# Kernel optimization log

Measured on AMD Instinct MI355X. Metric: run time of the kernel, lower is better.

The kernel has to match this reference:

```python
import math
import jax, jax.numpy as jnp
import numpy as np

WH, WW = 7, 7
NUM_HEADS = 16


def _relative_position_index(wh, ww):
    # Static int index table, identical to the torch buffer construction.
    ch, cw = np.arange(wh), np.arange(ww)
    coords = np.stack(np.meshgrid(ch, cw, indexing='ij'))        # (2, wh, ww)
    cf = coords.reshape(2, -1)                                    # (2, N)
    rel = cf[:, :, None] - cf[:, None, :]                         # (2, N, N)
    rel = rel.transpose(1, 2, 0).copy()                           # (N, N, 2)
    rel[:, :, 0] += wh - 1
    rel[:, :, 1] += ww - 1
    rel[:, :, 0] *= 2 * ww - 1
    return rel.sum(-1)                                            # (N, N) int


def setup_inputs() -> dict:
    key = jax.random.key(0)
    ks = jax.random.split(key, 7)
    B_, N, C = 2048, WH * WW, 512
    nW = 64
    s = 1.0 / math.sqrt(C)
    return {
        'x': jax.random.normal(ks[0], (B_, N, C), jnp.float32),
        'mask': jax.random.normal(ks[1], (nW, N, N), jnp.float32),
        'qkv_w': jax.random.normal(ks[2], (3 * C, C), jnp.float32) * s,
        'qkv_b': jax.random.normal(ks[3], (3 * C,), jnp.float32) * 0.02,
        'proj_w': jax.random.normal(ks[4], (C, C), jnp.float32) * s,
        'proj_b': jax.random.normal(ks[5], (C,), jnp.float32) * 0.02,
        'bias_table': jax.random.normal(ks[6], (2 * WH - 1, 2 * WW - 1, NUM_HEADS), jnp.float32) * 0.02,
    }


def reference(x, mask, qkv_w, qkv_b, proj_w, proj_b, bias_table):
    B_, N, C = x.shape
    nH = NUM_HEADS
    hd = C // nH
    scale = math.sqrt(hd)  # self.scale = qk_scale or sqrt(head_dim)

    qkv = x @ qkv_w.T + qkv_b                                   # (B_, N, 3C)
    qkv = qkv.reshape(B_, N, 3, nH, hd).transpose(2, 0, 3, 1, 4)  # (3, B_, nH, N, hd)
    q, k, v = qkv[0], qkv[1], qkv[2]

    attn = jnp.einsum('bhnd,bhmd->bhnm', q, k) / scale           # (B_, nH, N, N)

    idx = _relative_position_index(WH, WW).reshape(-1)            # (N*N,) static
    bias = bias_table.reshape(-1, nH)[idx].reshape(N, N, nH)      # gather
    attn = attn + bias.transpose(2, 0, 1)[None]                   # (B_, nH, N, N)

    nW = mask.shape[0]
    attn = attn.reshape(B_ // nW, nW, nH, N, N) + mask[None, :, None]
    attn = attn.reshape(B_, nH, N, N)

    attn = jax.nn.softmax(attn, axis=-1)
    out = jnp.einsum('bhnm,bhmd->bhnd', attn, v)                  # (B_, nH, N, hd)
    out = out.transpose(0, 2, 1, 3).reshape(B_, N, C)
    return out @ proj_w.T + proj_b
```

## Files before the change

### kernel.cpp

```cpp
#include <hip/hip_runtime.h>
#include <hip/hip_bf16.h>


typedef __bf16  bf16x8 __attribute__((ext_vector_type(8)));
typedef float   f32x4  __attribute__((ext_vector_type(4)));

#define B_TOT   2048
#define NTOK    49
#define CDIM    512
#define NHEAD   16
#define HDIM    32
#define MROWS   (B_TOT * NTOK)
#define QKVN    (3 * CDIM)

__device__ __forceinline__ void load_lds16(const void* gptr, void* lptr) {
    __builtin_amdgcn_global_load_lds(
        (const __attribute__((address_space(1))) unsigned int*)gptr,
        (__attribute__((address_space(3))) unsigned int*)lptr,
        16, 0, 0);
}
__device__ __forceinline__ void load_lds4(const void* gptr, void* lptr) {
    __builtin_amdgcn_global_load_lds(
        (const __attribute__((address_space(1))) unsigned int*)gptr,
        (__attribute__((address_space(3))) unsigned int*)lptr,
        4, 0, 0);
}

__global__ void cvt_f32_bf16(const float* __restrict__ in,
                             __hip_bfloat16* __restrict__ out, int n4) {
    int idx = blockIdx.x * blockDim.x + threadIdx.x;
    int stride = gridDim.x * blockDim.x;
    for (int i = idx; i < n4; i += stride) {
        float4 f = ((const float4*)in)[i];
        union { __hip_bfloat16 h[4]; ushort4 u; } c;
        c.h[0] = __float2bfloat16(f.x);
        c.h[1] = __float2bfloat16(f.y);
        c.h[2] = __float2bfloat16(f.z);
        c.h[3] = __float2bfloat16(f.w);
        ((ushort4*)out)[i] = c.u;
    }
}

template <typename OutT>
__global__ __launch_bounds__(256) void gemm_bt(
    const __hip_bfloat16* __restrict__ A,
    const __hip_bfloat16* __restrict__ B,
    const float* __restrict__ bias,
    OutT* __restrict__ C,
    int M, int N, int K)
{
    __shared__ __align__(16) __hip_bfloat16 As[128 * 32];
    __shared__ __align__(16) __hip_bfloat16 Bs[128 * 32];

    const int tid  = threadIdx.x;
    const int lane = tid & 63;
    const int wave = tid >> 6;
    const int wm   = (wave >> 1) * 64;
    const int wn   = (wave & 1) * 64;
    const int quad = lane >> 4;
    const int l16  = lane & 15;

    const int m0 = blockIdx.y * 128;
    const int n0 = blockIdx.x * 128;

    const int off0 = tid * 8;
    const int off1 = (256 + tid) * 8;
    const int r0 = off0 >> 5, c0 = off0 & 31;
    const int r1 = off1 >> 5, c1 = off1 & 31;

    const __hip_bfloat16* Ab = A + (long)m0 * K;
    const __hip_bfloat16* Bb = B + (long)n0 * K;

    f32x4 acc[4][4] = {};

    for (int k0 = 0; k0 < K; k0 += 32) {
        load_lds16(Ab + (long)r0 * K + k0 + c0, &As[off0]);
        load_lds16(Ab + (long)r1 * K + k0 + c1, &As[off1]);
        load_lds16(Bb + (long)r0 * K + k0 + c0, &Bs[off0]);
        load_lds16(Bb + (long)r1 * K + k0 + c1, &Bs[off1]);
        __syncthreads();

        bf16x8 a[4], b[4];
#pragma unroll
        for (int i = 0; i < 4; ++i)
            a[i] = *(const bf16x8*)&As[(wm + i * 16 + l16) * 32 + quad * 8];
#pragma unroll
        for (int j = 0; j < 4; ++j)
            b[j] = *(const bf16x8*)&Bs[(wn + j * 16 + l16) * 32 + quad * 8];
#pragma unroll
        for (int i = 0; i < 4; ++i)
#pragma unroll
            for (int j = 0; j < 4; ++j)
                acc[i][j] = __builtin_amdgcn_mfma_f32_16x16x32_bf16(
                    a[i], b[j], acc[i][j], 0, 0, 0);
        __syncthreads();
    }

#pragma unroll
    for (int i = 0; i < 4; ++i) {
#pragma unroll
        for (int j = 0; j < 4; ++j) {
            const int col = n0 + wn + j * 16 + l16;
            const float bv = bias[col];
#pragma unroll
            for (int r = 0; r < 4; ++r) {
                const int row = m0 + wm + i * 16 + quad * 4 + r;
                const float val = acc[i][j][r] + bv;
                if constexpr (sizeof(OutT) == 2)
                    C[(long)row * N + col] = __float2bfloat16(val);
                else
                    C[(long)row * N + col] = val;
            }
        }
    }
}

#define QS_OFF   0
#define KS_OFF   12544
#define VS_OFF   25088
#define BIAS_OFF 41472
#define MASK_OFF 42824
#define SMEM_BYTES 52432

__global__ __launch_bounds__(256) void attn_mfma(
    const __hip_bfloat16* __restrict__ qkv,
    const float* __restrict__ mask,
    const float* __restrict__ bias_table,
    __hip_bfloat16* __restrict__ out)
{
    __shared__ __align__(16) char smem[SMEM_BYTES];

    const int tid  = threadIdx.x;
    const int lane = tid & 63;
    const int w    = tid >> 6;
    const int l16  = lane & 15;
    const int quad = lane >> 4;
    const int b    = blockIdx.x >> 2;
    const int hq   = blockIdx.x & 3;

    {
        const long rowbase = (long)b * NTOK * QKVN;
        for (int e = tid; e < 2352; e += 256) {
            const int m   = e / 784;
            const int rr  = e - m * 784;
            const int tok = rr >> 4, seg = rr & 15;
            const int segl = seg ^ (tok & 7);
            const __hip_bfloat16* src =
                qkv + rowbase + (long)tok * QKVN + m * 512 + hq * 128 + segl * 8;
            load_lds16(src, smem + e * 16);
        }
        for (int e = tid; e < 960; e += 256)
            ((unsigned int*)(smem + VS_OFF + 49 * 256))[e] = 0u;
        const float* msrc = mask + (long)(b & 63) * (NTOK * NTOK);
        for (int e = tid; e < NTOK * NTOK; e += 256)
            load_lds4(msrc + e, smem + MASK_OFF + e * 4);
        __hip_bfloat16* sb = (__hip_bfloat16*)(smem + BIAS_OFF);
        for (int e = tid; e < 676; e += 256) {
            const int w2 = e / 169, rel = e - w2 * 169;
            sb[e] = __float2bfloat16(bias_table[rel * NHEAD + hq * 4 + w2]);
        }
    }
    __syncthreads();

    const int fro = (w * 64 + quad * 16) ^ ((l16 & 7) << 4);
    bf16x8 af[4], bf[4];
#pragma unroll
    for (int t = 0; t < 4; ++t) {
        const int tok = t * 16 + l16;
        af[t] = *(const bf16x8*)(smem + KS_OFF + tok * 256 + fro);
        bf[t] = *(const bf16x8*)(smem + QS_OFF + tok * 256 + fro);
    }
    f32x4 acc[4][4] = {};
#pragma unroll
    for (int i = 0; i < 4; ++i)
#pragma unroll
        for (int j = 0; j < 4; ++j)
            acc[i][j] = __builtin_amdgcn_mfma_f32_16x16x32_bf16(
                af[i], bf[j], acc[i][j], 0, 0, 0);
    __syncthreads();

    const float scale = 0.17677669529663687f;
    const float* smf = (const float*)(smem + MASK_OFF);
    const __hip_bfloat16* sb = (const __hip_bfloat16*)(smem + BIAS_OFF);
    const int quad4 = quad * 4;

    int kp[4][4];
#pragma unroll
    for (int i = 0; i < 4; ++i)
#pragma unroll
        for (int r = 0; r < 4; ++r) {
            const int k  = i * 16 + quad4 + r;
            const int rj = k / 7, cj = k - rj * 7;
            kp[i][r] = (6 - rj) * 13 + (6 - cj);
        }

    char* pbase = smem + w * 6272;
#pragma unroll
    for (int j = 0; j < 4; ++j) {
        const int q   = j * 16 + l16;
        const bool qok = q < NTOK;
        const int ri  = q / 7, ci = q - ri * 7;
        const int qp  = ri * 13 + ci;
        const int mrow = q * NTOK;
        float mx = -1e30f;
#pragma unroll
        for (int i = 0; i < 4; ++i)
#pragma unroll
            for (int r = 0; r < 4; ++r) {
                const int k = i * 16 + quad4 + r;
                float v;
                if (qok && k < NTOK) {
                    v = fmaf(acc[i][j][r], scale,
                             __bfloat162float(sb[w * 169 + qp + kp[i][r]]) + smf[mrow + k]);
                } else {
                    v = -1e30f;
                }
                acc[i][j][r] = v;
                mx = fmaxf(mx, v);
            }
        mx = fmaxf(mx, __shfl_xor(mx, 16));
        mx = fmaxf(mx, __shfl_xor(mx, 32));
        float s = 0.f;
#pragma unroll
        for (int i = 0; i < 4; ++i)
#pragma unroll
            for (int r = 0; r < 4; ++r) {
                const float ev = __expf(acc[i][j][r] - mx);
                acc[i][j][r] = ev;
                s += ev;
            }
        s += __shfl_xor(s, 16);
        s += __shfl_xor(s, 32);
        const float inv = 1.0f / s;
        if (qok) {
            char* prow = pbase + q * 128;
            const int xr = (q & 7) << 4;
#pragma unroll
            for (int i = 0; i < 4; ++i) {
                union { __hip_bfloat16 h[4]; uint2 u; } pk;
#pragma unroll
                for (int r = 0; r < 4; ++r)
                    pk.h[r] = __float2bfloat16(acc[i][j][r] * inv);
                *(uint2*)(prow + ((i * 32 + quad * 8) ^ xr)) = pk.u;
            }
        }
    }
    __syncthreads();

    bf16x8 pa[4][2];
#pragma unroll
    for (int mt = 0; mt < 4; ++mt) {
        const int q  = mt * 16 + l16;
        const int xr = (q & 7) << 4;
#pragma unroll
        for (int ks = 0; ks < 2; ++ks)
            pa[mt][ks] = *(const bf16x8*)(pbase + q * 128 + ((ks * 64 + quad * 16) ^ xr));
    }
    bf16x8 vb[2][2];
#pragma unroll
    for (int dt = 0; dt < 2; ++dt)
#pragma unroll
        for (int ks = 0; ks < 2; ++ks)
#pragma unroll
            for (int e = 0; e < 8; ++e) {
                const int key = ks * 32 + quad * 8 + e;
                const int dby = (w * 32 + dt * 16 + l16) * 2;
                vb[dt][ks][e] = *(const __bf16*)(smem + VS_OFF + key * 256 + (dby ^ (e << 4)));
            }
    f32x4 o[4][2] = {};
#pragma unroll
    for (int mt = 0; mt < 4; ++mt)
#pragma unroll
        for (int dt = 0; dt < 2; ++dt)
#pragma unroll
            for (int ks = 0; ks < 2; ++ks)
                o[mt][dt] = __builtin_amdgcn_mfma_f32_16x16x32_bf16(
                    pa[mt][ks], vb[dt][ks], o[mt][dt], 0, 0, 0);

    const long obase = (long)b * NTOK * CDIM + hq * 128 + w * 32;
#pragma unroll
    for (int mt = 0; mt < 4; ++mt)
#pragma unroll
        for (int r = 0; r < 4; ++r) {
            const int q = mt * 16 + quad4 + r;
            if (q < NTOK) {
                const long rb = obase + (long)q * CDIM;
#pragma unroll
                for (int dt = 0; dt < 2; ++dt)
                    out[rb + dt * 16 + l16] = __float2bfloat16(o[mt][dt][r]);
            }
        }
}

extern "C" void kernel_launch(void* const* d_in, const int* in_sizes, int n_in,
                              void* d_out, int out_size, void* d_ws, size_t ws_size,
                              hipStream_t stream) {
    const float* x          = (const float*)d_in[0];
    const float* mask       = (const float*)d_in[1];
    const float* qkv_w      = (const float*)d_in[2];
    const float* qkv_b      = (const float*)d_in[3];
    const float* proj_w     = (const float*)d_in[4];
    const float* proj_b     = (const float*)d_in[5];
    const float* bias_table = (const float*)d_in[6];

    char* ws = (char*)d_ws;
    __hip_bfloat16* xb   = (__hip_bfloat16*)(ws);
    __hip_bfloat16* qw   = (__hip_bfloat16*)(ws + 102760448);
    __hip_bfloat16* pw   = (__hip_bfloat16*)(ws + 104333312);
    __hip_bfloat16* qkvb = (__hip_bfloat16*)(ws + 104857600);
    __hip_bfloat16* ao   = xb;

    cvt_f32_bf16<<<32768, 256, 0, stream>>>(x, xb, (MROWS * CDIM) / 4);
    cvt_f32_bf16<<<768,   256, 0, stream>>>(qkv_w, qw, (QKVN * CDIM) / 4);
    cvt_f32_bf16<<<256,   256, 0, stream>>>(proj_w, pw, (CDIM * CDIM) / 4);

    gemm_bt<__hip_bfloat16><<<dim3(QKVN / 128, MROWS / 128), 256, 0, stream>>>(
        xb, qw, qkv_b, qkvb, MROWS, QKVN, CDIM);

    attn_mfma<<<B_TOT * 4, 256, 0, stream>>>(qkvb, mask, bias_table, ao);

    gemm_bt<float><<<dim3(CDIM / 128, MROWS / 128), 256, 0, stream>>>(
        ao, pw, proj_b, (float*)d_out, MROWS, CDIM, CDIM);
}
```

Baseline: 795.4 us.

## Replace GEMM with 256x256-tile, double-buffered, ping-pong scheduled MFMA kernel

Replaces the 128x128 single-buffered GEMM with a 512-thread kernel that computes 256x256 tiles over K-steps of 64. Global-to-LDS loads are split into half-tiles and staged into a double buffer, interleaved with MFMA phases using explicit vmcnt waits, barriers and setprio so loads overlap compute. Block IDs are swizzled across 8 groups for L2 locality, and the kernel uses 128KB of dynamic LDS. The aim is less barrier and load stall time and more data reuse per tile, at the cost of high register and LDS use (two blocks per CU) and fragile hand-written wait counts.

```diff
diff --git a/kernel.cpp b/kernel.cpp
--- a/kernel.cpp
+++ b/kernel.cpp
@@ -41,75 +41,151 @@
     }
 }
 
+#define BARR    asm volatile("s_barrier" ::: "memory")
+#define WAITV(N) asm volatile("s_waitcnt vmcnt(" #N ")" ::: "memory")
+#define MFMA16(av, bv, cv) __builtin_amdgcn_mfma_f32_16x16x32_bf16(av, bv, cv, 0, 0, 0)
+
 template <typename OutT>
-__global__ __launch_bounds__(256) void gemm_bt(
+__global__ __launch_bounds__(512, 2) void gemm256(
     const __hip_bfloat16* __restrict__ A,
     const __hip_bfloat16* __restrict__ B,
     const float* __restrict__ bias,
     OutT* __restrict__ C,
-    int M, int N, int K)
+    int M, int N, int K, int nbx, int cpx)
 {
-    __shared__ __align__(16) __hip_bfloat16 As[128 * 32];
-    __shared__ __align__(16) __hip_bfloat16 Bs[128 * 32];
+    extern __shared__ __align__(16) char smem[];
+    char* sA = smem;
+    char* sB = smem + 65536;
+
+    const int NT = K >> 6;
 
     const int tid  = threadIdx.x;
     const int lane = tid & 63;
     const int wave = tid >> 6;
-    const int wm   = (wave >> 1) * 64;
-    const int wn   = (wave & 1) * 64;
+    const int wm   = wave >> 2;
+    const int wn   = wave & 3;
+    const int l16  = lane & 15;
     const int quad = lane >> 4;
-    const int l16  = lane & 15;
-
-    const int m0 = blockIdx.y * 128;
-    const int n0 = blockIdx.x * 128;
-
-    const int off0 = tid * 8;
-    const int off1 = (256 + tid) * 8;
-    const int r0 = off0 >> 5, c0 = off0 & 31;
-    const int r1 = off1 >> 5, c1 = off1 & 31;
-
-    const __hip_bfloat16* Ab = A + (long)m0 * K;
-    const __hip_bfloat16* Bb = B + (long)n0 * K;
-
-    f32x4 acc[4][4] = {};
-
-    for (int k0 = 0; k0 < K; k0 += 32) {
-        load_lds16(Ab + (long)r0 * K + k0 + c0, &As[off0]);
-        load_lds16(Ab + (long)r1 * K + k0 + c1, &As[off1]);
-        load_lds16(Bb + (long)r0 * K + k0 + c0, &Bs[off0]);
-        load_lds16(Bb + (long)r1 * K + k0 + c1, &Bs[off1]);
-        __syncthreads();
-
-        bf16x8 a[4], b[4];
-#pragma unroll
-        for (int i = 0; i < 4; ++i)
-            a[i] = *(const bf16x8*)&As[(wm + i * 16 + l16) * 32 + quad * 8];
-#pragma unroll
-        for (int j = 0; j < 4; ++j)
-            b[j] = *(const bf16x8*)&Bs[(wn + j * 16 + l16) * 32 + quad * 8];
-#pragma unroll
-        for (int i = 0; i < 4; ++i)
-#pragma unroll
-            for (int j = 0; j < 4; ++j)
-                acc[i][j] = __builtin_amdgcn_mfma_f32_16x16x32_bf16(
-                    a[i], b[j], acc[i][j], 0, 0, 0);
-        __syncthreads();
-    }
-
-#pragma unroll
-    for (int i = 0; i < 4; ++i) {
-#pragma unroll
-        for (int j = 0; j < 4; ++j) {
-            const int col = n0 + wn + j * 16 + l16;
+
+    const int id = blockIdx.x;
+    const int sw = (id & 7) * cpx + (id >> 3);
+    const int mb = sw / nbx;
+    const int nb = sw - mb * nbx;
+    const int m0 = mb << 8;
+    const int n0 = nb << 8;
+
+    const int r  = tid >> 2;
+    const int ch = tid & 3;
+    const __hip_bfloat16* Ag0 = A + (size_t)(m0 + r) * K + ch * 8;
+    const __hip_bfloat16* Ag1 = Ag0 + (size_t)128 * K;
+    const __hip_bfloat16* Bg0 = B + (size_t)(n0 + r) * K + ch * 8;
+    const __hip_bfloat16* Bg1 = Bg0 + (size_t)128 * K;
+    char* dA = sA + tid * 16;
+    char* dB = sB + tid * 16;
+
+#define STAGE_A(t2, kh) \
+    { load_lds16(Ag0 + (t2) * 64 + (kh) * 32, dA + ((t2) & 1) * 32768 + (kh) * 16384);        \
+      load_lds16(Ag1 + (t2) * 64 + (kh) * 32, dA + ((t2) & 1) * 32768 + (kh) * 16384 + 8192); }
+#define STAGE_B(t2, kh) \
+    { load_lds16(Bg0 + (t2) * 64 + (kh) * 32, dB + ((t2) & 1) * 32768 + (kh) * 16384);        \
+      load_lds16(Bg1 + (t2) * 64 + (kh) * 32, dB + ((t2) & 1) * 32768 + (kh) * 16384 + 8192); }
+
+    STAGE_A(0, 0); STAGE_B(0, 0);
+    STAGE_A(0, 1); STAGE_B(0, 1);
+    STAGE_A(1, 0); STAGE_B(1, 0);
+    WAITV(8);
+    BARR;
+
+    const int tA = (wm * 128 + l16) * 64 + quad * 16;
+    const int tB = (wn * 64  + l16) * 64 + quad * 16;
+
+    f32x4 acc[8][4] = {};
+    bf16x8 a[8], b[2];
+
+#pragma unroll 2
+    for (int t = 0; t < NT; ++t) {
+        const int sl = (t & 1) * 32768;
+        const char* pA0 = sA + sl;
+        const char* pB0 = sB + sl;
+        const char* pA1 = sA + sl + 16384;
+        const char* pB1 = sB + sl + 16384;
+
+#pragma unroll
+        for (int i = 0; i < 8; ++i) a[i] = *(const bf16x8*)(pA0 + tA + i * 1024);
+        b[0] = *(const bf16x8*)(pB0 + tB);
+        b[1] = *(const bf16x8*)(pB0 + tB + 1024);
+        if (t + 1 < NT) STAGE_A(t + 1, 1);
+        BARR;
+        __builtin_amdgcn_s_setprio(1);
+#pragma unroll
+        for (int i = 0; i < 8; ++i) {
+            acc[i][0] = MFMA16(a[i], b[0], acc[i][0]);
+            acc[i][1] = MFMA16(a[i], b[1], acc[i][1]);
+        }
+        __builtin_amdgcn_s_setprio(0);
+        BARR;
+
+        b[0] = *(const bf16x8*)(pB0 + tB + 2048);
+        b[1] = *(const bf16x8*)(pB0 + tB + 3072);
+        if (t + 1 < NT) STAGE_B(t + 1, 1);
+        BARR;
+        __builtin_amdgcn_s_setprio(1);
+#pragma unroll
+        for (int i = 0; i < 8; ++i) {
+            acc[i][2] = MFMA16(a[i], b[0], acc[i][2]);
+            acc[i][3] = MFMA16(a[i], b[1], acc[i][3]);
+        }
+        __builtin_amdgcn_s_setprio(0);
+        if (t < NT - 1) { WAITV(8); } else { WAITV(0); }
+        BARR;
+
+#pragma unroll
+        for (int i = 0; i < 8; ++i) a[i] = *(const bf16x8*)(pA1 + tA + i * 1024);
+        b[0] = *(const bf16x8*)(pB1 + tB);
+        b[1] = *(const bf16x8*)(pB1 + tB + 1024);
+        if (t + 2 < NT) STAGE_A(t + 2, 0);
+        BARR;
+        __builtin_amdgcn_s_setprio(1);
+#pragma unroll
+        for (int i = 0; i < 8; ++i) {
+            acc[i][0] = MFMA16(a[i], b[0], acc[i][0]);
+            acc[i][1] = MFMA16(a[i], b[1], acc[i][1]);
+        }
+        __builtin_amdgcn_s_setprio(0);
+        BARR;
+
+        b[0] = *(const bf16x8*)(pB1 + tB + 2048);
+        b[1] = *(const bf16x8*)(pB1 + tB + 3072);
+        if (t + 2 < NT) STAGE_B(t + 2, 0);
+        BARR;
+        __builtin_amdgcn_s_setprio(1);
+#pragma unroll
+        for (int i = 0; i < 8; ++i) {
+            acc[i][2] = MFMA16(a[i], b[0], acc[i][2]);
+            acc[i][3] = MFMA16(a[i], b[1], acc[i][3]);
+        }
+        __builtin_amdgcn_s_setprio(0);
+        if (t < NT - 2) { WAITV(8); }
+        else if (t == NT - 2) { WAITV(4); }
+        BARR;
+    }
+#undef STAGE_A
+#undef STAGE_B
+
+#pragma unroll
+    for (int i = 0; i < 8; ++i) {
+#pragma unroll
+        for (int jj = 0; jj < 4; ++jj) {
+            const int col = n0 + wn * 64 + jj * 16 + l16;
             const float bv = bias[col];
 #pragma unroll
-            for (int r = 0; r < 4; ++r) {
-                const int row = m0 + wm + i * 16 + quad * 4 + r;
-                const float val = acc[i][j][r] + bv;
+            for (int rr = 0; rr < 4; ++rr) {
+                const int row = m0 + wm * 128 + i * 16 + quad * 4 + rr;
+                const float val = acc[i][jj][rr] + bv;
                 if constexpr (sizeof(OutT) == 2)
-                    C[(long)row * N + col] = __float2bfloat16(val);
+                    C[(size_t)row * N + col] = __float2bfloat16(val);
                 else
-                    C[(long)row * N + col] = val;
+                    C[(size_t)row * N + col] = val;
             }
         }
     }
@@ -310,15 +386,26 @@
     __hip_bfloat16* qkvb = (__hip_bfloat16*)(ws + 104857600);
     __hip_bfloat16* ao   = xb;
 
+    static int attr_done = 0;
+    if (!attr_done) {
+        hipFuncSetAttribute(
+            reinterpret_cast<const void*>(&gemm256<__hip_bfloat16>),
+            hipFuncAttributeMaxDynamicSharedMemorySize, 131072);
+        hipFuncSetAttribute(
+            reinterpret_cast<const void*>(&gemm256<float>),
+            hipFuncAttributeMaxDynamicSharedMemorySize, 131072);
+        attr_done = 1;
+    }
+
     cvt_f32_bf16<<<32768, 256, 0, stream>>>(x, xb, (MROWS * CDIM) / 4);
     cvt_f32_bf16<<<768,   256, 0, stream>>>(qkv_w, qw, (QKVN * CDIM) / 4);
     cvt_f32_bf16<<<256,   256, 0, stream>>>(proj_w, pw, (CDIM * CDIM) / 4);
 
-    gemm_bt<__hip_bfloat16><<<dim3(QKVN / 128, MROWS / 128), 256, 0, stream>>>(
-        xb, qw, qkv_b, qkvb, MROWS, QKVN, CDIM);
+    gemm256<__hip_bfloat16><<<2352, 512, 131072, stream>>>(
+        xb, qw, qkv_b, qkvb, MROWS, QKVN, CDIM, 6, 294);
 
     attn_mfma<<<B_TOT * 4, 256, 0, stream>>>(qkvb, mask, bias_table, ao);
 
-    gemm_bt<float><<<dim3(CDIM / 128, MROWS / 128), 256, 0, stream>>>(
-        ao, pw, proj_b, (float*)d_out, MROWS, CDIM, CDIM);
-}
+    gemm256<float><<<784, 512, 131072, stream>>>(
+        ao, pw, proj_b, (float*)d_out, MROWS, CDIM, CDIM, 2, 98);
+}
```

Result: faster. 774.2 us (-2.7%).

## Rewrite GEMM with double-buffered K=64 tiles, swizzled LDS, and XCD-aware block remap

Applied to the files above, without the earlier changes.

Replaces the simple single-buffer GEMM with a version that stages 64-wide K tiles into double-buffered LDS, with an XOR swizzle to avoid bank conflicts. Global-to-LDS loads for the next tiles are interleaved with MFMA work using manual waitcnt, barriers and s_setprio. Blocks move to a 1D grid with a remap that groups consecutive tiles per XCD for L2 locality. This adds complex hand-managed synchronization that risks subtle ordering bugs.

```diff
diff --git a/kernel.cpp b/kernel.cpp
--- a/kernel.cpp
+++ b/kernel.cpp
@@ -41,75 +41,136 @@
     }
 }
 
+#define BARR    asm volatile("s_barrier" ::: "memory")
+#define WAITV(N) asm volatile("s_waitcnt vmcnt(" #N ")" ::: "memory")
+#define LGKM0   asm volatile("s_waitcnt lgkmcnt(0)" ::: "memory")
+#define MFMA16(av, bv, cv) __builtin_amdgcn_mfma_f32_16x16x32_bf16(av, bv, cv, 0, 0, 0)
+
 template <typename OutT>
-__global__ __launch_bounds__(256) void gemm_bt(
+__global__ __launch_bounds__(256, 2) void gemm128(
     const __hip_bfloat16* __restrict__ A,
     const __hip_bfloat16* __restrict__ B,
     const float* __restrict__ bias,
     OutT* __restrict__ C,
-    int M, int N, int K)
+    int M, int N, int K, int nbx, int cpx)
 {
-    __shared__ __align__(16) __hip_bfloat16 As[128 * 32];
-    __shared__ __align__(16) __hip_bfloat16 Bs[128 * 32];
+    __shared__ __align__(16) char smem[65536];
+    char* sA = smem;
+    char* sB = smem + 32768;
+
+    const int NT = K >> 6;
 
     const int tid  = threadIdx.x;
     const int lane = tid & 63;
     const int wave = tid >> 6;
-    const int wm   = (wave >> 1) * 64;
-    const int wn   = (wave & 1) * 64;
+    const int wm2  = wave >> 1;
+    const int wn2  = wave & 1;
+    const int l16  = lane & 15;
     const int quad = lane >> 4;
-    const int l16  = lane & 15;
-
-    const int m0 = blockIdx.y * 128;
-    const int n0 = blockIdx.x * 128;
-
-    const int off0 = tid * 8;
-    const int off1 = (256 + tid) * 8;
-    const int r0 = off0 >> 5, c0 = off0 & 31;
-    const int r1 = off1 >> 5, c1 = off1 & 31;
-
-    const __hip_bfloat16* Ab = A + (long)m0 * K;
-    const __hip_bfloat16* Bb = B + (long)n0 * K;
-
+
+    const int id = blockIdx.x;
+    const int sw = (id & 7) * cpx + (id >> 3);
+    const int mb = sw / nbx;
+    const int nb = sw - mb * nbx;
+    const int m0 = mb << 7;
+    const int n0 = nb << 7;
+
+    const int srow = tid >> 3;
+    const int scg  = (((tid & 7) ^ (srow & 7)) << 3);
+    const __hip_bfloat16* Asrc = A + (size_t)(m0 + srow) * K + scg;
+    const __hip_bfloat16* Bsrc = B + (size_t)(n0 + srow) * K + scg;
+    char* dA = sA + tid * 16;
+    char* dB = sB + tid * 16;
+
+#define STG_A(t2) { const int sl_ = ((t2) & 1) * 16384;                     \
+    load_lds16(Asrc + (t2) * 64,                    dA + sl_);              \
+    load_lds16(Asrc + (size_t)32 * K + (t2) * 64,   dA + sl_ + 4096);       \
+    load_lds16(Asrc + (size_t)64 * K + (t2) * 64,   dA + sl_ + 8192);       \
+    load_lds16(Asrc + (size_t)96 * K + (t2) * 64,   dA + sl_ + 12288); }
+#define STG_B(t2) { const int sl_ = ((t2) & 1) * 16384;                     \
+    load_lds16(Bsrc + (t2) * 64,                    dB + sl_);              \
+    load_lds16(Bsrc + (size_t)32 * K + (t2) * 64,   dB + sl_ + 4096);       \
+    load_lds16(Bsrc + (size_t)64 * K + (t2) * 64,   dB + sl_ + 8192);       \
+    load_lds16(Bsrc + (size_t)96 * K + (t2) * 64,   dB + sl_ + 12288); }
+
+    STG_A(0); STG_B(0); STG_A(1);
+    WAITV(4);
+    BARR;
+
+    const int rbA = (wm2 * 64 + l16) * 128;
+    const int rbB = (wn2 * 64 + l16) * 128;
+    const int c0 = (quad * 16) ^ ((l16 & 7) << 4);
+    const int c1 = c0 ^ 64;
+
+    bf16x8 ar[8], br[4], br2[4];
     f32x4 acc[4][4] = {};
 
-    for (int k0 = 0; k0 < K; k0 += 32) {
-        load_lds16(Ab + (long)r0 * K + k0 + c0, &As[off0]);
-        load_lds16(Ab + (long)r1 * K + k0 + c1, &As[off1]);
-        load_lds16(Bb + (long)r0 * K + k0 + c0, &Bs[off0]);
-        load_lds16(Bb + (long)r1 * K + k0 + c1, &Bs[off1]);
-        __syncthreads();
-
-        bf16x8 a[4], b[4];
-#pragma unroll
-        for (int i = 0; i < 4; ++i)
-            a[i] = *(const bf16x8*)&As[(wm + i * 16 + l16) * 32 + quad * 8];
-#pragma unroll
-        for (int j = 0; j < 4; ++j)
-            b[j] = *(const bf16x8*)&Bs[(wn + j * 16 + l16) * 32 + quad * 8];
-#pragma unroll
-        for (int i = 0; i < 4; ++i)
-#pragma unroll
-            for (int j = 0; j < 4; ++j)
-                acc[i][j] = __builtin_amdgcn_mfma_f32_16x16x32_bf16(
-                    a[i], b[j], acc[i][j], 0, 0, 0);
-        __syncthreads();
-    }
-
-#pragma unroll
-    for (int i = 0; i < 4; ++i) {
-#pragma unroll
-        for (int j = 0; j < 4; ++j) {
-            const int col = n0 + wn + j * 16 + l16;
+#pragma unroll 2
+    for (int t = 0; t < NT; ++t) {
+        const int sl = (t & 1) * 16384;
+        const char* pA = sA + sl + rbA;
+        const char* pB = sB + sl + rbB;
+
+#pragma unroll
+        for (int mf = 0; mf < 4; ++mf) {
+            ar[2 * mf]     = *(const bf16x8*)(pA + mf * 2048 + c0);
+            ar[2 * mf + 1] = *(const bf16x8*)(pA + mf * 2048 + c1);
+        }
+#pragma unroll
+        for (int nf = 0; nf < 2; ++nf) {
+            br[2 * nf]     = *(const bf16x8*)(pB + nf * 2048 + c0);
+            br[2 * nf + 1] = *(const bf16x8*)(pB + nf * 2048 + c1);
+        }
+        if (t + 1 < NT) STG_B(t + 1);
+        BARR; LGKM0;
+        __builtin_amdgcn_s_setprio(1);
+#pragma unroll
+        for (int mf = 0; mf < 4; ++mf)
+#pragma unroll
+            for (int nf = 0; nf < 2; ++nf) {
+                acc[mf][nf] = MFMA16(ar[2 * mf],     br[2 * nf],     acc[mf][nf]);
+                acc[mf][nf] = MFMA16(ar[2 * mf + 1], br[2 * nf + 1], acc[mf][nf]);
+            }
+        __builtin_amdgcn_s_setprio(0);
+        BARR;
+
+#pragma unroll
+        for (int nf = 0; nf < 2; ++nf) {
+            br2[2 * nf]     = *(const bf16x8*)(pB + (2 + nf) * 2048 + c0);
+            br2[2 * nf + 1] = *(const bf16x8*)(pB + (2 + nf) * 2048 + c1);
+        }
+        if (t + 2 < NT) STG_A(t + 2);
+        BARR; LGKM0;
+        __builtin_amdgcn_s_setprio(1);
+#pragma unroll
+        for (int mf = 0; mf < 4; ++mf)
+#pragma unroll
+            for (int nf = 0; nf < 2; ++nf) {
+                acc[mf][2 + nf] = MFMA16(ar[2 * mf],     br2[2 * nf],     acc[mf][2 + nf]);
+                acc[mf][2 + nf] = MFMA16(ar[2 * mf + 1], br2[2 * nf + 1], acc[mf][2 + nf]);
+            }
+        __builtin_amdgcn_s_setprio(0);
+        if (t + 2 < NT)      { WAITV(4); }
+        else if (t + 1 < NT) { WAITV(0); }
+        BARR;
+    }
+#undef STG_A
+#undef STG_B
+
+#pragma unroll
+    for (int mf = 0; mf < 4; ++mf) {
+#pragma unroll
+        for (int nf = 0; nf < 4; ++nf) {
+            const int col = n0 + wn2 * 64 + nf * 16 + l16;
             const float bv = bias[col];
 #pragma unroll
-            for (int r = 0; r < 4; ++r) {
-                const int row = m0 + wm + i * 16 + quad * 4 + r;
-                const float val = acc[i][j][r] + bv;
+            for (int rr = 0; rr < 4; ++rr) {
+                const int row = m0 + wm2 * 64 + mf * 16 + quad * 4 + rr;
+                const float val = acc[mf][nf][rr] + bv;
                 if constexpr (sizeof(OutT) == 2)
-                    C[(long)row * N + col] = __float2bfloat16(val);
+                    C[(size_t)row * N + col] = __float2bfloat16(val);
                 else
-                    C[(long)row * N + col] = val;
+                    C[(size_t)row * N + col] = val;
             }
         }
     }
@@ -314,11 +375,11 @@
     cvt_f32_bf16<<<768,   256, 0, stream>>>(qkv_w, qw, (QKVN * CDIM) / 4);
     cvt_f32_bf16<<<256,   256, 0, stream>>>(proj_w, pw, (CDIM * CDIM) / 4);
 
-    gemm_bt<__hip_bfloat16><<<dim3(QKVN / 128, MROWS / 128), 256, 0, stream>>>(
-        xb, qw, qkv_b, qkvb, MROWS, QKVN, CDIM);
+    gemm128<__hip_bfloat16><<<9408, 256, 0, stream>>>(
+        xb, qw, qkv_b, qkvb, MROWS, QKVN, CDIM, 12, 1176);
 
     attn_mfma<<<B_TOT * 4, 256, 0, stream>>>(qkvb, mask, bias_table, ao);
 
-    gemm_bt<float><<<dim3(CDIM / 128, MROWS / 128), 256, 0, stream>>>(
-        ao, pw, proj_b, (float*)d_out, MROWS, CDIM, CDIM);
-}
+    gemm128<float><<<3136, 256, 0, stream>>>(
+        ao, pw, proj_b, (float*)d_out, MROWS, CDIM, CDIM, 4, 392);
+}
```

Measured after the change: 748.7 us. 5.9% less time.
